# Performance work log

Measured on AMD Instinct MI355X. Metric: run time of the kernel, lower is better.

The kernel has to match this reference:

```python
import jax, jax.numpy as jnp
import numpy as np
from jax import lax

# ---- configuration (matches init_kwargs) ----
B, C_DATA, C_FEAT, H, W = 2, 8, 8, 160, 160
K = 7                      # number of soft nearest neighbors
PS, STRIDE, WIN = 10, 5, 15
FEAT, C_EMB = 64, 8
N1 = (H - PS) // STRIDE + 1   # 31, no padding needed
N2 = (W - PS) // STRIDE + 1   # 31
NEG_INF = -1e9


def _conv3(x, w, b):
    y = lax.conv_general_dilated(x, w, (1, 1), 'SAME',
                                 dimension_numbers=('NCHW', 'OIHW', 'NCHW'))
    return y + b[None, :, None, None]


def _cnn(x, w1, b1, w2, b2, w3, b3):
    # depth-3 DnCNN-style net: conv-relu-conv-relu-conv (bn=False, lastact=linear)
    h = jax.nn.relu(_conv3(x, w1, b1))
    h = jax.nn.relu(_conv3(h, w2, b2))
    return _conv3(h, w3, b3)


def _im2patch(x):
    # x: [b,c,H,W] -> [b,n1,n2,c*PS*PS]; patch flattened channel-major (c,p1,p2)
    ii = jnp.arange(N1)[:, None] * STRIDE + jnp.arange(PS)[None, :]  # [n1,PS]
    jj = jnp.arange(N2)[:, None] * STRIDE + jnp.arange(PS)[None, :]  # [n2,PS]
    p = x[:, :, ii[:, None, :, None], jj[None, :, None, :]]  # [b,c,n1,n2,PS,PS]
    p = jnp.transpose(p, (0, 2, 3, 1, 4, 5))
    return p.reshape(p.shape[0], N1, N2, -1)


def _n3block(x_data, x_faet, ew1, eb1, ew2, eb2, ew3, eb3,
             tw1, tb1, tw2, tb2, tw3, tb3):
    xe = _cnn(x_faet, ew1, eb1, ew2, eb2, ew3, eb3)      # [b,8,H,W] embeddings
    log_temp = _cnn(x_faet, tw1, tb1, tw2, tb2, tw3, tb3)  # [b,1,H,W]

    ye = _im2patch(xe)                        # [b,n1,n2,E]; queries == database
    yp = _im2patch(x_data)                    # [b,n1,n2,F]
    lt = _im2patch(log_temp).mean(-1)         # scalar log-temp per patch
    temp = jnp.exp(lt)[..., None]             # [b,n1,n2,1] (temp_bias = 1)

    S = min(WIN, N1, N2)
    R = S // 2
    base1 = jnp.clip(jnp.arange(N1) - R, 0, N1 - S)   # clamped window top-left
    base2 = jnp.clip(jnp.arange(N2) - R, 0, N2 - S)
    offs = jnp.stack(jnp.meshgrid(jnp.arange(S), jnp.arange(S), indexing='ij'),
                     axis=-1).reshape(-1, 2)          # [S*S,2]
    i1, i2 = jnp.arange(N1), jnp.arange(N2)
    yn = jnp.sum(ye * ye, axis=-1)            # [b,n1,n2] squared norms

    @jax.checkpoint
    def dist_step(carry, off):
        j1 = base1 + off[0]
        j2 = base2 + off[1]
        xs = ye[:, j1][:, :, j2]              # [b,n1,n2,E] candidate embedding
        xn = yn[:, j1][:, :, j2]
        dot = jnp.einsum('bije,bije->bij', ye, xs)
        d = yn + xn - 2.0 * dot               # squared euclidean distance
        self_m = (j1 == i1)[:, None] & (j2 == i2)[None, :]
        return carry, (d, self_m)

    _, (D, selfm) = lax.scan(dist_step, None, offs)
    D = jnp.moveaxis(D, 0, -1)                # [b,n1,n2,O], O=S*S
    selfm = jnp.moveaxis(selfm, 0, -1)        # [n1,n2,O]

    logits = -D / temp
    logits = jnp.where(selfm, NEG_INF, logits)   # exclude_self

    # continuous deterministic top-k (N3Net): w_j = softmax(a); a += log(1 - w_j)
    ws = []
    for _ in range(K):
        wgt = jax.nn.softmax(logits, axis=-1)
        ws.append(wgt)
        logits = logits + jnp.log1p(-jnp.minimum(wgt, 1.0 - 1e-6))
    Wk = jnp.stack(ws, axis=-1)               # [b,n1,n2,O,K]

    @jax.checkpoint
    def agg_step(z, args):
        off, wk = args                        # wk: [b,n1,n2,K]
        j1 = base1 + off[0]
        j2 = base2 + off[1]
        ys = yp[:, j1][:, :, j2]              # [b,n1,n2,F]
        return z + wk[..., :, None] * ys[..., None, :], None

    z0 = jnp.zeros(yp.shape[:3] + (K, yp.shape[-1]), yp.dtype)
    z, _ = lax.scan(agg_step, z0, (offs, jnp.moveaxis(Wk, 3, 0)))
    z = z - yp[..., None, :]                  # residue=True
    out_p = jnp.concatenate([yp[..., None, :], z], axis=3)  # [b,n1,n2,K+1,F]

    # fold patch volumes back to image, averaging overlaps
    b = out_p.shape[0]
    C = (K + 1) * C_DATA
    out_p = out_p.reshape(b, N1, N2, K + 1, C_DATA, PS, PS)
    out_p = jnp.transpose(out_p, (0, 3, 4, 1, 2, 5, 6)).reshape(b, C, N1, N2, PS, PS)
    rows = jnp.arange(N1)[:, None] * STRIDE + jnp.arange(PS)[None, :]
    cols = jnp.arange(N2)[:, None] * STRIDE + jnp.arange(PS)[None, :]
    lin = (rows[:, None, :, None] * W + cols[None, :, None, :]).reshape(-1)
    vals = out_p.reshape(b, C, -1)
    img = jnp.zeros((b, C, H * W), out_p.dtype).at[:, :, lin].add(vals)
    cnt = jnp.zeros((H * W,), out_p.dtype).at[lin].add(1.0)
    return (img / cnt).reshape(b, C, H, W)


def setup_inputs() -> dict:
    key = jax.random.key(0)
    ks = jax.random.split(key, 8)
    f32 = jnp.float32
    wn = lambda k, s: jax.random.normal(k, s, f32) * 0.05
    return dict(
        x_data=jax.random.normal(ks[0], (B, C_DATA, H, W), f32),
        x_faet=jax.random.normal(ks[1], (B, C_FEAT, H, W), f32),
        ew1=wn(ks[2], (FEAT, C_FEAT, 3, 3)), eb1=jnp.zeros((FEAT,), f32),
        ew2=wn(ks[3], (FEAT, FEAT, 3, 3)), eb2=jnp.zeros((FEAT,), f32),
        ew3=wn(ks[4], (C_EMB, FEAT, 3, 3)), eb3=jnp.zeros((C_EMB,), f32),
        tw1=wn(ks[5], (FEAT, C_FEAT, 3, 3)), tb1=jnp.zeros((FEAT,), f32),
        tw2=wn(ks[6], (FEAT, FEAT, 3, 3)), tb2=jnp.zeros((FEAT,), f32),
        tw3=wn(ks[7], (1, FEAT, 3, 3)), tb3=jnp.zeros((1,), f32),
    )


def reference(x_data, x_faet, ew1, eb1, ew2, eb2, ew3, eb3,
              tw1, tb1, tw2, tb2, tw3, tb3):
    return _n3block(x_data, x_faet, ew1, eb1, ew2, eb2, ew3, eb3,
                    tw1, tb1, tw2, tb2, tw3, tb3)
```

## Files before the change

kernel.cpp:

```cpp
#include <hip/hip_runtime.h>
#include <math.h>

#define BN 2
#define HH 160
#define WW 160
#define CDATA 8
#define PS 10
#define STR 5
#define N1 31
#define N2 31
#define NSITE (N1*N2)
#define SITES (BN*NSITE)
#define SWIN 15
#define NOFF 225
#define KK 7
#define EDIM 800
#define NPIX 25600
#define LP 40
#define KP 480
#define COLP 992
#define GP 34
#define KSPLIT 5

typedef __attribute__((ext_vector_type(8))) short s8v;
typedef __attribute__((ext_vector_type(8))) unsigned short u8v;
typedef __attribute__((ext_vector_type(4))) float f4v;

__device__ __forceinline__ unsigned short f2bf(float f) {
    unsigned u = __float_as_uint(f);
    return (unsigned short)((u + 0x7FFFu + ((u >> 16) & 1u)) >> 16);
}
__device__ __forceinline__ float bf2f(unsigned short h) {
    return __uint_as_float(((unsigned)h) << 16);
}

__device__ __forceinline__ float block_sum(float v, float* sred) {
    #pragma unroll
    for (int o = 32; o; o >>= 1) v += __shfl_xor(v, o);
    __syncthreads();
    if ((threadIdx.x & 63) == 0) sred[threadIdx.x >> 6] = v;
    __syncthreads();
    return sred[0] + sred[1] + sred[2] + sred[3];
}

__global__ __launch_bounds__(256) void prep_k(const float* __restrict__ xd,
                                              const float* __restrict__ ew2,
                                              const float* __restrict__ tw2,
                                              const float* __restrict__ ew1,
                                              const float* __restrict__ tw1,
                                              const float* __restrict__ ew3,
                                              const float* __restrict__ tw3,
                                              unsigned short* __restrict__ ypT,
                                              unsigned short* __restrict__ wp,
                                              unsigned short* __restrict__ wp1,
                                              unsigned short* __restrict__ wp3) {
    int blk = blockIdx.x;
    int t = threadIdx.x;
    if (blk < 1600) {
        int b = blk / 800, e = blk % 800;
        int cd = e & 7, pp = e >> 3;
        int pi = pp / 10, pj = pp % 10;
        const float* src = xd + ((size_t)(b * 8 + cd) * HH + pi) * WW + pj;
        unsigned short* dst = ypT + (size_t)blk * COLP;
        for (int it = 0; it < 4; ++it) {
            int col = it * 256 + t;
            if (col < COLP) {
                int j1 = col >> 5, j2 = col & 31;
                unsigned short v = 0;
                if (j2 < 31) v = f2bf(src[(j1 * 5) * WW + j2 * 5]);
                dst[col] = v;
            }
        }
    } else if (blk < 1888) {
        int idx = (blk - 1600) * 256 + t;
        int which = idx / (64 * 576); int r = idx % (64 * 576);
        int n = r / 576, k = r % 576;
        int p = k / 64, c = k % 64;
        const float* w = which ? tw2 : ew2;
        wp[idx] = f2bf(w[(n * 64 + c) * 9 + p]);
    } else if (blk < 1936) {
        int idx = (blk - 1888) * 256 + t;
        if (idx < 128 * 96) {
            int n = idx / 96, k = idx % 96;
            int tap = k >> 3, c = k & 7;
            unsigned short v = 0;
            if (tap < 9) {
                const float* w = (n < 64) ? ew1 : tw1;
                v = f2bf(w[((n & 63) * 8 + c) * 9 + tap]);
            }
            wp1[idx] = v;
        }
    } else {
        int idx = (blk - 1936) * 256 + t;
        if (idx < 2 * 16 * 576) {
            int which = idx / (16 * 576); int r = idx % (16 * 576);
            int n = r / 576, k = r % 576;
            int tap = k / 64, c = k % 64;
            float w = 0.f; bool lo = false;
            if (which == 0) { w = ew3[((n & 7) * 64 + c) * 9 + tap]; lo = (n >= 8); }
            else if (n < 2) { w = tw3[c * 9 + tap]; lo = (n == 1); }
            unsigned short hi = f2bf(w);
            wp3[idx] = lo ? f2bf(w - bf2f(hi)) : hi;
            if (which == 1 && n >= 2) wp3[idx] = 0;
        }
    }
}

__global__ __launch_bounds__(256) void conv1_mfma_k(const float* __restrict__ xf,
                                                    const unsigned short* __restrict__ wp1,
                                                    const float* __restrict__ eb1,
                                                    const float* __restrict__ tb1,
                                                    unsigned short* __restrict__ h1) {
    __shared__ unsigned short Al[128 * LP];
    __shared__ unsigned short Bl[64 * LP];
    const int t = threadIdx.x;
    const int m0 = blockIdx.x * 64;
    const int wv = t >> 6, lane = t & 63;
    f4v acc[2][4];
    #pragma unroll
    for (int fj = 0; fj < 2; ++fj)
        #pragma unroll
        for (int fi = 0; fi < 4; ++fi) { f4v z = {0.f,0.f,0.f,0.f}; acc[fj][fi] = z; }
    const int mp = m0 + (t >> 2);
    const int b = mp / NPIX, rp = mp % NPIX;
    const int py = rp / WW, px = rp % WW;
    for (int ks = 0; ks < 3; ++ks) {
        int tap = ks * 4 + (t & 3);
        int dy = tap / 3 - 1, dx = tap % 3 - 1;
        int yy = py + dy, xx = px + dx;
        bool ok = (tap < 9) && yy >= 0 && yy < HH && xx >= 0 && xx < WW;
        u8v bv;
        #pragma unroll
        for (int c = 0; c < 8; ++c)
            bv[c] = ok ? f2bf(xf[((size_t)(b * 8 + c)) * NPIX + yy * WW + xx]) : 0;
        __syncthreads();
        *(u8v*)(Bl + (t >> 2) * LP + (t & 3) * 8) = bv;
        #pragma unroll
        for (int it = 0; it < 2; ++it) {
            int idx = t + it * 256;
            int row = idx >> 2, seg = idx & 3;
            *(u8v*)(Al + row * LP + seg * 8) = *(const u8v*)(wp1 + row * 96 + ks * 32 + seg * 8);
        }
        __syncthreads();
        s8v af[2], bf[4];
        #pragma unroll
        for (int fj = 0; fj < 2; ++fj)
            af[fj] = *(const s8v*)((const short*)Al + (wv * 32 + fj * 16 + (lane & 15)) * LP + (lane >> 4) * 8);
        #pragma unroll
        for (int fi = 0; fi < 4; ++fi)
            bf[fi] = *(const s8v*)((const short*)Bl + (fi * 16 + (lane & 15)) * LP + (lane >> 4) * 8);
        #pragma unroll
        for (int fj = 0; fj < 2; ++fj)
            #pragma unroll
            for (int fi = 0; fi < 4; ++fi)
                acc[fj][fi] = __builtin_amdgcn_mfma_f32_16x16x32_bf16(af[fj], bf[fi], acc[fj][fi], 0, 0, 0);
    }
    #pragma unroll
    for (int fj = 0; fj < 2; ++fj) {
        int nb = wv * 32 + fj * 16 + (lane >> 4) * 4;
        float bias4[4];
        #pragma unroll
        for (int c = 0; c < 4; ++c) {
            int n = nb + c;
            bias4[c] = (n < 64) ? eb1[n] : tb1[n - 64];
        }
        #pragma unroll
        for (int fi = 0; fi < 4; ++fi) {
            int mm = m0 + fi * 16 + (lane & 15);
            ushort4 o;
            o.x = f2bf(fmaxf(acc[fj][fi][0] + bias4[0], 0.f));
            o.y = f2bf(fmaxf(acc[fj][fi][1] + bias4[1], 0.f));
            o.z = f2bf(fmaxf(acc[fj][fi][2] + bias4[2], 0.f));
            o.w = f2bf(fmaxf(acc[fj][fi][3] + bias4[3], 0.f));
            *(ushort4*)(h1 + (size_t)mm * 128 + nb) = o;
        }
    }
}

__global__ __launch_bounds__(256) void conv2_mfma_k(const unsigned short* __restrict__ h1,
                                                    const unsigned short* __restrict__ wp,
                                                    const float* __restrict__ eb2,
                                                    const float* __restrict__ tb2,
                                                    unsigned short* __restrict__ h2) {
    __shared__ unsigned short Al[64 * LP];
    __shared__ unsigned short Bl[128 * LP];
    const int t = threadIdx.x;
    const int which = blockIdx.y;
    const int m0 = blockIdx.x * 128;
    const int wv = t >> 6, lane = t & 63;
    f4v acc[4][2];
    #pragma unroll
    for (int nf = 0; nf < 4; ++nf)
        #pragma unroll
        for (int mf = 0; mf < 2; ++mf) { f4v z = {0.f,0.f,0.f,0.f}; acc[nf][mf] = z; }
    const unsigned short* wb = wp + (size_t)which * 64 * 576;
    const int sm = t >> 2, sq = (t & 3) * 8;
    const int mp0 = m0 + sm;
    const int b0 = mp0 / NPIX, rp0 = mp0 % NPIX;
    const int py0 = rp0 / WW, px0 = rp0 % WW;
    const int mp1 = m0 + 64 + sm;
    const int b1_ = mp1 / NPIX, rp1 = mp1 % NPIX;
    const int py1 = rp1 / WW, px1 = rp1 % WW;
    for (int step = 0; step < 18; ++step) {
        const int p = step >> 1, ch = (step & 1) * 32;
        const int dy = p / 3 - 1, dx = p % 3 - 1;
        s8v av = *(const s8v*)(wb + sm * 576 + p * 64 + ch + sq);
        s8v bv0, bv1;
        #pragma unroll
        for (int j = 0; j < 8; j++) { bv0[j] = 0; bv1[j] = 0; }
        int yy = py0 + dy, xx = px0 + dx;
        if (yy >= 0 && yy < HH && xx >= 0 && xx < WW)
            bv0 = *(const s8v*)((const short*)h1 + ((size_t)b0 * NPIX + yy * WW + xx) * 128 + which * 64 + ch + sq);
        yy = py1 + dy; xx = px1 + dx;
        if (yy >= 0 && yy < HH && xx >= 0 && xx < WW)
            bv1 = *(const s8v*)((const short*)h1 + ((size_t)b1_ * NPIX + yy * WW + xx) * 128 + which * 64 + ch + sq);
        __syncthreads();
        *(s8v*)((short*)Al + sm * LP + sq) = av;
        *(s8v*)((short*)Bl + sm * LP + sq) = bv0;
        *(s8v*)((short*)Bl + (64 + sm) * LP + sq) = bv1;
        __syncthreads();
        s8v af[4], bf[2];
        #pragma unroll
        for (int nf = 0; nf < 4; ++nf)
            af[nf] = *(const s8v*)((const short*)Al + (nf * 16 + (lane & 15)) * LP + (lane >> 4) * 8);
        #pragma unroll
        for (int mf = 0; mf < 2; ++mf)
            bf[mf] = *(const s8v*)((const short*)Bl + (wv * 32 + mf * 16 + (lane & 15)) * LP + (lane >> 4) * 8);
        #pragma unroll
        for (int nf = 0; nf < 4; ++nf)
            #pragma unroll
            for (int mf = 0; mf < 2; ++mf)
                acc[nf][mf] = __builtin_amdgcn_mfma_f32_16x16x32_bf16(af[nf], bf[mf], acc[nf][mf], 0, 0, 0);
    }
    const float* bias = which ? tb2 : eb2;
    #pragma unroll
    for (int nf = 0; nf < 4; ++nf) {
        int nb = nf * 16 + (lane >> 4) * 4;
        f4v bv4 = *(const f4v*)(bias + nb);
        #pragma unroll
        for (int mf = 0; mf < 2; ++mf) {
            int mm = m0 + wv * 32 + mf * 16 + (lane & 15);
            ushort4 o;
            o.x = f2bf(fmaxf(acc[nf][mf][0] + bv4[0], 0.f));
            o.y = f2bf(fmaxf(acc[nf][mf][1] + bv4[1], 0.f));
            o.z = f2bf(fmaxf(acc[nf][mf][2] + bv4[2], 0.f));
            o.w = f2bf(fmaxf(acc[nf][mf][3] + bv4[3], 0.f));
            *(ushort4*)(h2 + ((size_t)which * 51200 + mm) * 64 + nb) = o;
        }
    }
}

__global__ __launch_bounds__(256) void conv3_mfma_k(const unsigned short* __restrict__ h2,
                                                    const unsigned short* __restrict__ wp3,
                                                    const float* __restrict__ eb3,
                                                    const float* __restrict__ tb3,
                                                    float* __restrict__ xe,
                                                    float* __restrict__ ltm) {
    __shared__ unsigned short Al[16 * LP];
    __shared__ unsigned short Bl[128 * LP];
    const int t = threadIdx.x;
    const int which = blockIdx.y;
    const int m0 = blockIdx.x * 128;
    const int wv = t >> 6, lane = t & 63;
    f4v acc[2];
    { f4v z = {0.f,0.f,0.f,0.f}; acc[0] = z; acc[1] = z; }
    const unsigned short* wb = wp3 + (size_t)which * 16 * 576;
    const int sm = t >> 2, sq = (t & 3) * 8;
    const int mp0 = m0 + sm;
    const int b0 = mp0 / NPIX, rp0 = mp0 % NPIX;
    const int py0 = rp0 / WW, px0 = rp0 % WW;
    const int mp1 = m0 + 64 + sm;
    const int b1_ = mp1 / NPIX, rp1 = mp1 % NPIX;
    const int py1 = rp1 / WW, px1 = rp1 % WW;
    for (int step = 0; step < 18; ++step) {
        const int p = step >> 1, ch = (step & 1) * 32;
        const int dy = p / 3 - 1, dx = p % 3 - 1;
        s8v av;
        if (t < 64) av = *(const s8v*)(wb + (t >> 2) * 576 + p * 64 + ch + (t & 3) * 8);
        s8v bv0, bv1;
        #pragma unroll
        for (int j = 0; j < 8; j++) { bv0[j] = 0; bv1[j] = 0; }
        int yy = py0 + dy, xx = px0 + dx;
        if (yy >= 0 && yy < HH && xx >= 0 && xx < WW)
            bv0 = *(const s8v*)((const short*)h2 + ((size_t)which * 51200 + (size_t)b0 * NPIX + yy * WW + xx) * 64 + ch + sq);
        yy = py1 + dy; xx = px1 + dx;
        if (yy >= 0 && yy < HH && xx >= 0 && xx < WW)
            bv1 = *(const s8v*)((const short*)h2 + ((size_t)which * 51200 + (size_t)b1_ * NPIX + yy * WW + xx) * 64 + ch + sq);
        __syncthreads();
        if (t < 64) *(s8v*)((short*)Al + (t >> 2) * LP + (t & 3) * 8) = av;
        *(s8v*)((short*)Bl + sm * LP + sq) = bv0;
        *(s8v*)((short*)Bl + (64 + sm) * LP + sq) = bv1;
        __syncthreads();
        s8v af = *(const s8v*)((const short*)Al + (lane & 15) * LP + (lane >> 4) * 8);
        #pragma unroll
        for (int mf = 0; mf < 2; ++mf) {
            s8v bf = *(const s8v*)((const short*)Bl + (wv * 32 + mf * 16 + (lane & 15)) * LP + (lane >> 4) * 8);
            acc[mf] = __builtin_amdgcn_mfma_f32_16x16x32_bf16(af, bf, acc[mf], 0, 0, 0);
        }
    }
    #pragma unroll
    for (int mf = 0; mf < 2; ++mf) {
        int mm = m0 + wv * 32 + mf * 16 + (lane & 15);
        if (which == 0) {
            f4v hilo;
            #pragma unroll
            for (int c = 0; c < 4; ++c)
                hilo[c] = acc[mf][c] + __shfl_xor(acc[mf][c], 32);
            if (lane < 32) {
                int nb = (lane >> 4) * 4;
                f4v o;
                #pragma unroll
                for (int c = 0; c < 4; ++c) o[c] = hilo[c] + eb3[nb + c];
                *(f4v*)(xe + (size_t)mm * 8 + nb) = o;
            }
        } else {
            if ((lane >> 4) == 0)
                ltm[mm] = acc[mf][0] + acc[mf][1] + tb3[0];
        }
    }
}

__global__ __launch_bounds__(256) void im2patch_k(const float* __restrict__ xe,
                                                  const float* __restrict__ ltm,
                                                  unsigned short* __restrict__ yeH,
                                                  unsigned short* __restrict__ yeL,
                                                  float* __restrict__ yn,
                                                  float* __restrict__ tempv) {
    __shared__ float sred[4];
    int site = blockIdx.x;
    int b = site / NSITE; int ij = site % NSITE;
    int i1 = ij / N2, i2 = ij % N2;
    int t = threadIdx.x;
    const float* xeb = xe + (size_t)b * NPIX * 8;
    float ssq = 0.f;
    for (int e = t; e < EDIM; e += 256) {
        int rr = e / 80, rem = e % 80;
        float v = xeb[((size_t)(i1 * STR + rr) * WW + i2 * STR) * 8 + rem];
        unsigned short h = f2bf(v);
        float lo = v - bf2f(h);
        yeH[(size_t)site * EDIM + e] = h;
        yeL[(size_t)site * EDIM + e] = f2bf(lo);
        ssq += v * v;
    }
    float tot = block_sum(ssq, sred);
    if (t == 0) yn[site] = tot;
    float sl = 0.f;
    if (t < 100) {
        int rr = t / 10, q = t % 10;
        sl = ltm[(size_t)b * NPIX + (i1 * STR + rr) * WW + (i2 * STR + q)];
    }
    float slt = block_sum(sl, sred);
    if (t == 0) tempv[site] = expf(slt * (1.f / 100.f));
}

__global__ __launch_bounds__(256) void gram_mfma_k(const unsigned short* __restrict__ yeH,
                                                   const unsigned short* __restrict__ yeL,
                                                   float* __restrict__ dotsC) {
    __shared__ unsigned short AsH[32 * GP], AsL[32 * GP];
    __shared__ unsigned short BsH[256 * GP], BsL[256 * GP];
    int blk = blockIdx.x;
    int kc = blk % KSPLIT; int r = blk / KSPLIT;
    int nh = r & 1; r >>= 1;
    int b = r / N1, i1 = r % N1;
    int b1 = min(max(i1 - 7, 0), 16);
    int t = threadIdx.x;
    int wv = t >> 6, lane = t & 63;
    f4v acc[2][4];
    #pragma unroll
    for (int mt = 0; mt < 2; ++mt)
        #pragma unroll
        for (int nt = 0; nt < 4; ++nt) { f4v z = {0.f,0.f,0.f,0.f}; acc[mt][nt] = z; }
    const size_t abase = (size_t)((b * N1 + i1) * N2) * EDIM;
    for (int ks = kc * 5; ks < kc * 5 + 5; ++ks) {
        __syncthreads();
        {
            int idx = t & 127;
            int row = idx >> 2, seg = idx & 3;
            u8v v;
            #pragma unroll
            for (int u = 0; u < 8; ++u) v[u] = 0;
            if (row < 31)
                v = *(const u8v*)((t < 128 ? yeH : yeL) + abase + (size_t)row * EDIM + ks * 32 + seg * 8);
            *(u8v*)((t < 128 ? AsH : AsL) + row * GP + seg * 8) = v;
        }
        #pragma unroll
        for (int rep = 0; rep < 8; ++rep) {
            int idx = t + rep * 256;
            int isH = idx < 1024;
            int id2 = idx & 1023;
            int row = id2 >> 2, seg = id2 & 3;
            int dj = nh * 8 + (row >> 5), j2 = row & 31;
            u8v v;
            #pragma unroll
            for (int u = 0; u < 8; ++u) v[u] = 0;
            if (dj < 15 && j2 < 31) {
                size_t site = (size_t)((b * N1 + b1 + dj) * N2 + j2);
                v = *(const u8v*)((isH ? yeH : yeL) + site * EDIM + ks * 32 + seg * 8);
            }
            *(u8v*)((isH ? BsH : BsL) + row * GP + seg * 8) = v;
        }
        __syncthreads();
        s8v afH[2], afL[2], bfH[4], bfL[4];
        #pragma unroll
        for (int mt = 0; mt < 2; ++mt) {
            int ar = mt * 16 + (lane & 15);
            afH[mt] = *(const s8v*)((const short*)AsH + ar * GP + (lane >> 4) * 8);
            afL[mt] = *(const s8v*)((const short*)AsL + ar * GP + (lane >> 4) * 8);
        }
        #pragma unroll
        for (int nt = 0; nt < 4; ++nt) {
            int br = wv * 64 + nt * 16 + (lane & 15);
            bfH[nt] = *(const s8v*)((const short*)BsH + br * GP + (lane >> 4) * 8);
            bfL[nt] = *(const s8v*)((const short*)BsL + br * GP + (lane >> 4) * 8);
        }
        #pragma unroll
        for (int mt = 0; mt < 2; ++mt)
            #pragma unroll
            for (int nt = 0; nt < 4; ++nt) {
                acc[mt][nt] = __builtin_amdgcn_mfma_f32_16x16x32_bf16(afH[mt], bfH[nt], acc[mt][nt], 0, 0, 0);
                acc[mt][nt] = __builtin_amdgcn_mfma_f32_16x16x32_bf16(afH[mt], bfL[nt], acc[mt][nt], 0, 0, 0);
                acc[mt][nt] = __builtin_amdgcn_mfma_f32_16x16x32_bf16(afL[mt], bfH[nt], acc[mt][nt], 0, 0, 0);
            }
    }
    float* dk = dotsC + (size_t)kc * SITES * NOFF;
    #pragma unroll
    for (int mt = 0; mt < 2; ++mt) {
        int i2b = mt * 16 + (lane >> 4) * 4;
        #pragma unroll
        for (int nt = 0; nt < 4; ++nt) {
            int n = wv * 64 + nt * 16 + (lane & 15);
            int dj = nh * 8 + (n >> 5), j2 = n & 31;
            if (dj >= 15 || j2 >= 31) continue;
            #pragma unroll
            for (int c = 0; c < 4; ++c) {
                int i2 = i2b + c;
                if (i2 >= 31) continue;
                int b2 = min(max(i2 - 7, 0), 16);
                int dc = j2 - b2;
                if (dc < 0 || dc >= SWIN) continue;
                size_t site = (size_t)((b * N1 + i1) * N2 + i2);
                dk[site * NOFF + dj * SWIN + dc] = acc[mt][nt][c];
            }
        }
    }
}

__global__ __launch_bounds__(256) void softmax_k(const float* __restrict__ dotsC,
                                                 const float* __restrict__ yn,
                                                 const float* __restrict__ tempv,
                                                 float* __restrict__ wkout) {
    int wid = blockIdx.x * 4 + (threadIdx.x >> 6);
    if (wid >= SITES) return;
    int lane = threadIdx.x & 63;
    int b = wid / NSITE; int ij = wid % NSITE;
    int i1 = ij / N2, i2 = ij % N2;
    int b1 = min(max(i1 - 7, 0), 16);
    int b2 = min(max(i2 - 7, 0), 16);
    float yns = yn[wid];
    float tvi = 1.f / tempv[wid];
    float lg[4];
    #pragma unroll
    for (int r = 0; r < 4; ++r) {
        int t = lane + 64 * r;
        lg[r] = -1e9f;
        if (t < NOFF) {
            float dot = 0.f;
            #pragma unroll
            for (int kc = 0; kc < KSPLIT; ++kc)
                dot += dotsC[((size_t)kc * SITES + wid) * NOFF + t];
            int dj = t / SWIN, dc = t % SWIN;
            int j1 = b1 + dj, j2 = b2 + dc;
            float xn = yn[(b * N1 + j1) * N2 + j2];
            float d = yns + xn - 2.f * dot;
            lg[r] = -d * tvi;
            if (j1 == i1 && j2 == i2) lg[r] = -1e9f;
        }
    }
    float* wkr = wkout + (size_t)wid * (KK * NOFF);
    for (int k = 0; k < KK; ++k) {
        float m = fmaxf(fmaxf(lg[0], lg[1]), fmaxf(lg[2], lg[3]));
        #pragma unroll
        for (int o = 32; o; o >>= 1) m = fmaxf(m, __shfl_xor(m, o));
        float ex[4]; float s = 0.f;
        #pragma unroll
        for (int r = 0; r < 4; ++r) { ex[r] = expf(lg[r] - m); s += ex[r]; }
        #pragma unroll
        for (int o = 32; o; o >>= 1) s += __shfl_xor(s, o);
        float inv = 1.f / s;
        #pragma unroll
        for (int r = 0; r < 4; ++r) {
            float wgt = ex[r] * inv;
            int t = lane + 64 * r;
            if (t < NOFF) wkr[k * NOFF + t] = wgt;
            lg[r] += log1pf(-fminf(wgt, 1.f - 1e-6f));
        }
    }
}

__global__ __launch_bounds__(256) void abuild_k(const float* __restrict__ wk,
                                                unsigned short* __restrict__ Aglob) {
    int idx = blockIdx.x * 256 + threadIdx.x;
    if (idx >= 2 * 31 * 256 * 60) return;
    int kc8 = (idx % 60) * 8;
    int m   = (idx / 60) % 256;
    int i1  = (idx / (60 * 256)) % 31;
    int b   = idx / (60 * 256 * 31);
    int dj = kc8 >> 5, j2base = kc8 & 31;
    int pglob = m >> 4, slot = m & 15;
    int s = (slot >= 7) ? 1 : 0;
    int i2 = 2 * pglob + s;
    int k = slot - 7 * s;
    bool valid = (slot < 14) && (i2 <= 30);
    u8v o;
    #pragma unroll
    for (int u = 0; u < 8; ++u) o[u] = 0;
    if (valid) {
        int b2 = min(max(i2 - 7, 0), 16);
        int site = (b * N1 + i1) * N2 + i2;
        const float* wr = wk + (size_t)site * (KK * NOFF) + k * NOFF + dj * SWIN - b2;
        #pragma unroll
        for (int u = 0; u < 8; ++u) {
            int j2 = j2base + u;
            int dc = j2 - b2;
            if (j2 < 31 && dc >= 0 && dc < SWIN) o[u] = f2bf(wr[j2]);
        }
    }
    *(u8v*)(Aglob + (size_t)idx * 8) = o;
}

__global__ __launch_bounds__(256) void agg_gemm_k(const unsigned short* __restrict__ Aglob,
                                                  const unsigned short* __restrict__ ypT,
                                                  unsigned short* __restrict__ zbuf) {
    __shared__ unsigned short As[128 * 40];
    __shared__ unsigned short Bs[160 * 40];
    int blk = blockIdx.x;
    int b = blk / 310; int r = blk % 310;
    int i1 = r / 10; int r2 = r % 10;
    int mh = r2 / 5, nc = r2 % 5;
    int b1 = min(max(i1 - 7, 0), 16);
    int t = threadIdx.x;
    int wv = t >> 6, lane = t & 63;
    int wm = (wv & 1) * 64, we = (wv >> 1) * 80;
    const unsigned short* Ab = Aglob + ((size_t)(b * N1 + i1) * 256 + mh * 128) * KP;
    const unsigned short* Bb = ypT + ((size_t)b * 800 + nc * 160) * COLP + b1 * 32;
    f4v accr[4][5];
    #pragma unroll
    for (int mt = 0; mt < 4; ++mt)
        #pragma unroll
        for (int et = 0; et < 5; ++et) { f4v z = {0.f,0.f,0.f,0.f}; accr[mt][et] = z; }
    for (int ks = 0; ks < 15; ++ks) {
        __syncthreads();
        #pragma unroll
        for (int it = 0; it < 2; ++it) {
            int idx = t + it * 256;
            int row = idx >> 2, seg = idx & 3;
            *(u8v*)(As + row * 40 + seg * 8) = *(const u8v*)(Ab + (size_t)row * KP + ks * 32 + seg * 8);
        }
        #pragma unroll
        for (int it = 0; it < 3; ++it) {
            int idx = t + it * 256;
            if (idx < 640) {
                int row = idx >> 2, seg = idx & 3;
                *(u8v*)(Bs + row * 40 + seg * 8) = *(const u8v*)(Bb + (size_t)row * COLP + ks * 32 + seg * 8);
            }
        }
        __syncthreads();
        s8v af[4], bf[5];
        #pragma unroll
        for (int mt = 0; mt < 4; ++mt)
            af[mt] = *(const s8v*)((const short*)As + (wm + mt * 16 + (lane & 15)) * 40 + (lane >> 4) * 8);
        #pragma unroll
        for (int et = 0; et < 5; ++et)
            bf[et] = *(const s8v*)((const short*)Bs + (we + et * 16 + (lane & 15)) * 40 + (lane >> 4) * 8);
        #pragma unroll
        for (int mt = 0; mt < 4; ++mt)
            #pragma unroll
            for (int et = 0; et < 5; ++et)
                accr[mt][et] = __builtin_amdgcn_mfma_f32_16x16x32_bf16(af[mt], bf[et], accr[mt][et], 0, 0, 0);
    }
    unsigned short* zb = zbuf + ((size_t)(b * N1 + i1) * 256 + mh * 128) * 800 + nc * 160;
    #pragma unroll
    for (int mt = 0; mt < 4; ++mt) {
        int mrow = wm + mt * 16 + (lane >> 4) * 4;
        #pragma unroll
        for (int et = 0; et < 5; ++et) {
            int ecol = we + et * 16 + (lane & 15);
            #pragma unroll
            for (int c = 0; c < 4; ++c)
                zb[(size_t)(mrow + c) * 800 + ecol] = f2bf(accr[mt][et][c]);
        }
    }
}

__global__ __launch_bounds__(256) void finalize_k(const unsigned short* __restrict__ zbuf,
                                                  const float* __restrict__ xd,
                                                  float* __restrict__ out) {
    int pid = blockIdx.x * 256 + threadIdx.x;
    if (pid >= BN * NPIX) return;
    int b = pid / NPIX, pix = pid % NPIX;
    int h = pix / WW, w_ = pix % WW;
    int lo1 = max(0, (h - 5) / 5),  hi1 = min(30, h / 5);
    int lo2 = max(0, (w_ - 5) / 5), hi2 = min(30, w_ / 5);
    float cntinv = 1.f / (float)((hi1 - lo1 + 1) * (hi2 - lo2 + 1));
    float xv[8];
    #pragma unroll
    for (int cd = 0; cd < 8; ++cd) {
        xv[cd] = xd[((size_t)(b * 8 + cd)) * NPIX + pix];
        out[((size_t)(b * 64 + cd)) * NPIX + pix] = xv[cd];
    }
    for (int k = 0; k < KK; ++k) {
        float s[8];
        #pragma unroll
        for (int cd = 0; cd < 8; ++cd) s[cd] = 0.f;
        for (int i1 = lo1; i1 <= hi1; ++i1) {
            int pi = h - 5 * i1;
            for (int i2 = lo2; i2 <= hi2; ++i2) {
                int pj = w_ - 5 * i2;
                int m = 16 * (i2 >> 1) + k + 7 * (i2 & 1);
                const unsigned short* zp = zbuf + ((size_t)(b * N1 + i1) * 256 + m) * 800 + (pi * 10 + pj) * 8;
                u8v zv = *(const u8v*)zp;
                #pragma unroll
                for (int cd = 0; cd < 8; ++cd) s[cd] += bf2f(zv[cd]);
            }
        }
        #pragma unroll
        for (int cd = 0; cd < 8; ++cd)
            out[((size_t)(b * 64 + (k + 1) * 8 + cd)) * NPIX + pix] = s[cd] * cntinv - xv[cd];
    }
}

extern "C" void kernel_launch(void* const* d_in, const int* in_sizes, int n_in,
                              void* d_out, int out_size, void* d_ws, size_t ws_size,
                              hipStream_t stream) {
    (void)in_sizes; (void)n_in; (void)out_size; (void)ws_size;
    const float* x_data = (const float*)d_in[0];
    const float* x_faet = (const float*)d_in[1];
    const float* ew1 = (const float*)d_in[2];  const float* eb1 = (const float*)d_in[3];
    const float* ew2 = (const float*)d_in[4];  const float* eb2 = (const float*)d_in[5];
    const float* ew3 = (const float*)d_in[6];  const float* eb3 = (const float*)d_in[7];
    const float* tw1 = (const float*)d_in[8];  const float* tb1 = (const float*)d_in[9];
    const float* tw2 = (const float*)d_in[10]; const float* tb2 = (const float*)d_in[11];
    const float* tw3 = (const float*)d_in[12]; const float* tb3 = (const float*)d_in[13];
    float* out = (float*)d_out;

    char* base = (char*)d_ws;
    unsigned short* h1 = (unsigned short*)(base);
    unsigned short* h2 = (unsigned short*)(base + 13107200);
    unsigned short* wp1 = (unsigned short*)(base + 13107200);
    unsigned short* wp = (unsigned short*)(base + 26214400);
    float* yn    = (float*)(base + 26361856);
    float* tempv = (float*)(base + 26370048);
    unsigned short* ypT = (unsigned short*)(base + 26378240);
    float* xe    = (float*)(base + 29552640);
    float* ltm   = (float*)(base + 31191040);
    unsigned short* yeH = (unsigned short*)(base + 31395840);
    unsigned short* yeL = (unsigned short*)(base + 34471040);
    unsigned short* wp3 = (unsigned short*)(base + 37546240);
    unsigned short* Aglob = (unsigned short*)(base + 29552640);
    float* dotsC = (float*)h2;
    float* wkbuf = (float*)h1;
    unsigned short* zbuf = (unsigned short*)base;

    prep_k<<<2008, 256, 0, stream>>>(x_data, ew2, tw2, ew1, tw1, ew3, tw3, ypT, wp, wp1, wp3);
    conv1_mfma_k<<<800, 256, 0, stream>>>(x_faet, wp1, eb1, tb1, h1);
    conv2_mfma_k<<<dim3(400, 2), 256, 0, stream>>>(h1, wp, eb2, tb2, h2);
    conv3_mfma_k<<<dim3(400, 2), 256, 0, stream>>>(h2, wp3, eb3, tb3, xe, ltm);

    im2patch_k<<<BN * NSITE, 256, 0, stream>>>(xe, ltm, yeH, yeL, yn, tempv);
    gram_mfma_k<<<BN * N1 * 2 * KSPLIT, 256, 0, stream>>>(yeH, yeL, dotsC);
    softmax_k<<<(SITES + 3) / 4, 256, 0, stream>>>(dotsC, yn, tempv, wkbuf);

    abuild_k<<<(2 * 31 * 256 * 60) / 256, 256, 0, stream>>>(wkbuf, Aglob);
    agg_gemm_k<<<BN * 310, 256, 0, stream>>>(Aglob, ypT, zbuf);
    finalize_k<<<(BN * NPIX + 255) / 256, 256, 0, stream>>>(zbuf, x_data, out);
}
```

Measured before the change: 175.5 us.

## Fuse softmax weights with bf16 A-matrix construction to skip fp32 buffer

The softmax kernel now stages each iteration's weights in shared memory and writes the bf16 scattered A-matrix rows for the aggregation GEMM directly, including the zero-padding rows. This removes the separate abuild kernel and the round trip of the fp32 weight buffer (about 3 MB) through global memory. It also switches expf to the faster __expf intrinsic. In exchange it adds two block-wide barriers per k iteration and has inactive waves clamp their site index.

```diff
diff --git a/kernel.cpp b/kernel.cpp
--- a/kernel.cpp
+++ b/kernel.cpp
@@ -445,19 +445,23 @@
     }
 }
 
-__global__ __launch_bounds__(256) void softmax_k(const float* __restrict__ dotsC,
-                                                 const float* __restrict__ yn,
-                                                 const float* __restrict__ tempv,
-                                                 float* __restrict__ wkout) {
-    int wid = blockIdx.x * 4 + (threadIdx.x >> 6);
-    if (wid >= SITES) return;
-    int lane = threadIdx.x & 63;
-    int b = wid / NSITE; int ij = wid % NSITE;
+__global__ __launch_bounds__(256) void softmax_awrite_k(const float* __restrict__ dotsC,
+                                                        const float* __restrict__ yn,
+                                                        const float* __restrict__ tempv,
+                                                        unsigned short* __restrict__ Aglob) {
+    __shared__ float sw[4][228];
+    int wv = threadIdx.x >> 6, lane = threadIdx.x & 63;
+    int wid = blockIdx.x * 4 + wv;
+    bool active = (wid < SITES);
+    int wids = active ? wid : (SITES - 1);
+    int b = wids / NSITE; int ij = wids % NSITE;
     int i1 = ij / N2, i2 = ij % N2;
     int b1 = min(max(i1 - 7, 0), 16);
     int b2 = min(max(i2 - 7, 0), 16);
-    float yns = yn[wid];
-    float tvi = 1.f / tempv[wid];
+    int pglob = i2 >> 1, s = i2 & 1;
+    unsigned short* Abase = Aglob + (size_t)((b * N1 + i1) * 256) * KP;
+    float yns = yn[wids];
+    float tvi = 1.f / tempv[wids];
     float lg[4];
     #pragma unroll
     for (int r = 0; r < 4; ++r) {
@@ -467,7 +471,7 @@
             float dot = 0.f;
             #pragma unroll
             for (int kc = 0; kc < KSPLIT; ++kc)
-                dot += dotsC[((size_t)kc * SITES + wid) * NOFF + t];
+                dot += dotsC[((size_t)kc * SITES + wids) * NOFF + t];
             int dj = t / SWIN, dc = t % SWIN;
             int j1 = b1 + dj, j2 = b2 + dc;
             float xn = yn[(b * N1 + j1) * N2 + j2];
@@ -476,56 +480,50 @@
             if (j1 == i1 && j2 == i2) lg[r] = -1e9f;
         }
     }
-    float* wkr = wkout + (size_t)wid * (KK * NOFF);
     for (int k = 0; k < KK; ++k) {
         float m = fmaxf(fmaxf(lg[0], lg[1]), fmaxf(lg[2], lg[3]));
         #pragma unroll
         for (int o = 32; o; o >>= 1) m = fmaxf(m, __shfl_xor(m, o));
-        float ex[4]; float s = 0.f;
-        #pragma unroll
-        for (int r = 0; r < 4; ++r) { ex[r] = expf(lg[r] - m); s += ex[r]; }
-        #pragma unroll
-        for (int o = 32; o; o >>= 1) s += __shfl_xor(s, o);
-        float inv = 1.f / s;
+        float ex[4]; float ssum = 0.f;
+        #pragma unroll
+        for (int r = 0; r < 4; ++r) { ex[r] = __expf(lg[r] - m); ssum += ex[r]; }
+        #pragma unroll
+        for (int o = 32; o; o >>= 1) ssum += __shfl_xor(ssum, o);
+        float inv = 1.f / ssum;
         #pragma unroll
         for (int r = 0; r < 4; ++r) {
             float wgt = ex[r] * inv;
             int t = lane + 64 * r;
-            if (t < NOFF) wkr[k * NOFF + t] = wgt;
+            if (t < NOFF) sw[wv][t] = wgt;
             lg[r] += log1pf(-fminf(wgt, 1.f - 1e-6f));
         }
-    }
-}
-
-__global__ __launch_bounds__(256) void abuild_k(const float* __restrict__ wk,
-                                                unsigned short* __restrict__ Aglob) {
-    int idx = blockIdx.x * 256 + threadIdx.x;
-    if (idx >= 2 * 31 * 256 * 60) return;
-    int kc8 = (idx % 60) * 8;
-    int m   = (idx / 60) % 256;
-    int i1  = (idx / (60 * 256)) % 31;
-    int b   = idx / (60 * 256 * 31);
-    int dj = kc8 >> 5, j2base = kc8 & 31;
-    int pglob = m >> 4, slot = m & 15;
-    int s = (slot >= 7) ? 1 : 0;
-    int i2 = 2 * pglob + s;
-    int k = slot - 7 * s;
-    bool valid = (slot < 14) && (i2 <= 30);
-    u8v o;
-    #pragma unroll
-    for (int u = 0; u < 8; ++u) o[u] = 0;
-    if (valid) {
-        int b2 = min(max(i2 - 7, 0), 16);
-        int site = (b * N1 + i1) * N2 + i2;
-        const float* wr = wk + (size_t)site * (KK * NOFF) + k * NOFF + dj * SWIN - b2;
-        #pragma unroll
-        for (int u = 0; u < 8; ++u) {
-            int j2 = j2base + u;
-            int dc = j2 - b2;
-            if (j2 < 31 && dc >= 0 && dc < SWIN) o[u] = f2bf(wr[j2]);
-        }
-    }
-    *(u8v*)(Aglob + (size_t)idx * 8) = o;
+        __syncthreads();
+        if (active && lane < 60) {
+            u8v o;
+            #pragma unroll
+            for (int u = 0; u < 8; ++u) {
+                int n = lane * 8 + u;
+                int dj = n >> 5, j2 = n & 31;
+                int dc = j2 - b2;
+                o[u] = (j2 < 31 && dc >= 0 && dc < SWIN) ? f2bf(sw[wv][dj * SWIN + dc]) : (unsigned short)0;
+            }
+            int m_ = 16 * pglob + k + 7 * s;
+            *(u8v*)(Abase + (size_t)m_ * KP + lane * 8) = o;
+        }
+        __syncthreads();
+    }
+    if (active && s == 0 && lane < 60) {
+        u8v z;
+        #pragma unroll
+        for (int u = 0; u < 8; ++u) z[u] = 0;
+        *(u8v*)(Abase + (size_t)(16 * pglob + 14) * KP + lane * 8) = z;
+        *(u8v*)(Abase + (size_t)(16 * pglob + 15) * KP + lane * 8) = z;
+        if (i2 == 30) {
+            #pragma unroll
+            for (int sl = 7; sl < 14; ++sl)
+                *(u8v*)(Abase + (size_t)(16 * 15 + sl) * KP + lane * 8) = z;
+        }
+    }
 }
 
 __global__ __launch_bounds__(256) void agg_gemm_k(const unsigned short* __restrict__ Aglob,
@@ -658,7 +656,6 @@
     unsigned short* wp3 = (unsigned short*)(base + 37546240);
     unsigned short* Aglob = (unsigned short*)(base + 29552640);
     float* dotsC = (float*)h2;
-    float* wkbuf = (float*)h1;
     unsigned short* zbuf = (unsigned short*)base;
 
     prep_k<<<2008, 256, 0, stream>>>(x_data, ew2, tw2, ew1, tw1, ew3, tw3, ypT, wp, wp1, wp3);
@@ -668,9 +665,8 @@
 
     im2patch_k<<<BN * NSITE, 256, 0, stream>>>(xe, ltm, yeH, yeL, yn, tempv);
     gram_mfma_k<<<BN * N1 * 2 * KSPLIT, 256, 0, stream>>>(yeH, yeL, dotsC);
-    softmax_k<<<(SITES + 3) / 4, 256, 0, stream>>>(dotsC, yn, tempv, wkbuf);
-
-    abuild_k<<<(2 * 31 * 256 * 60) / 256, 256, 0, stream>>>(wkbuf, Aglob);
+    softmax_awrite_k<<<(SITES + 3) / 4, 256, 0, stream>>>(dotsC, yn, tempv, Aglob);
+
     agg_gemm_k<<<BN * 310, 256, 0, stream>>>(Aglob, ypT, zbuf);
     finalize_k<<<(BN * NPIX + 255) / 256, 256, 0, stream>>>(zbuf, x_data, out);
 }
```

Result: faster. 170.7 us (-2.7%).
